# Kernel optimization log

Measured on AMD Instinct MI355X. Metric: run time of the kernel, lower is better.

## Reference

```python
import jax, jax.numpy as jnp
import numpy as np

B, L, H, OUT = 128, 256, 512, 256


def setup_inputs() -> dict:
    key = jax.random.key(0)
    ks = jax.random.split(key, 13)
    s = 1.0 / np.sqrt(H)
    u = lambda k, shape: jax.random.uniform(k, shape, jnp.float32, -s, s)
    C = jax.random.normal(ks[0], (L, H), jnp.float32)
    # strictly increasing observation times per sample
    dt0 = jax.random.uniform(ks[1], (B, L, 1), jnp.float32)
    t = jnp.cumsum(dt0, axis=1)
    mask = jax.random.randint(ks[2], (B, L, H), 0, 2).astype(jnp.int32)
    # GRU-D parameters: fused gate weights [z | r | candidate]
    Wx = u(ks[3], (H, 3 * H))   # input -> gates
    Wh = u(ks[4], (H, 3 * H))   # hidden -> gates
    Wm = u(ks[5], (H, 3 * H))   # mask  -> gates
    b = u(ks[6], (3 * H,))
    w_gx = u(ks[7], (H,))       # diagonal input-decay weight
    b_gx = u(ks[8], (H,))
    W_gh = u(ks[9], (H, H))     # hidden-decay weight
    b_gh = u(ks[10], (H,))
    W_out = u(ks[11], (H, OUT))
    b_out = u(ks[12], (OUT,))
    return dict(C=C, t=t, mask=mask, Wx=Wx, Wh=Wh, Wm=Wm, b=b, w_gx=w_gx,
                b_gx=b_gx, W_gh=W_gh, b_gh=b_gh, W_out=W_out, b_out=b_out)


def _grud_decode(C, t, mask_f, Wx, Wh, Wm, b, w_gx, b_gx, W_gh, b_gh, W_out, b_out):
    Bn, Ln = t.shape[0], t.shape[1]
    Hn = C.shape[1]
    m = mask_f                                                     # (B,L,H) float 0/1
    tt = jnp.broadcast_to(t[:, :, 0:1], (Bn, Ln, Hn))              # (B,L,H)
    dt = tt - jnp.concatenate([tt[:, :1], tt[:, :-1]], axis=1)     # dt[:,0]=0
    x = jnp.broadcast_to(C[None], (Bn, Ln, Hn))
    # empirical mean of observed values per sample/feature
    x_mean = jnp.sum(m * x, axis=1) / jnp.maximum(jnp.sum(m, axis=1), 1.0)  # (B,H)

    def step(carry, inp):
        h, x_last, d_prev, m_prev = carry
        xi, mi, dti = inp                                          # xi:(H,), mi/dti:(B,H)
        # time since last observation (GRU-D delta recurrence)
        delta = dti + (1.0 - m_prev) * d_prev
        gamma_x = jnp.exp(-jnp.maximum(0.0, w_gx * delta + b_gx))  # input decay
        gamma_h = jnp.exp(-jnp.maximum(0.0, delta @ W_gh + b_gh))  # hidden decay
        x_hat = mi * xi + (1.0 - mi) * (gamma_x * x_last + (1.0 - gamma_x) * x_mean)
        h = gamma_h * h
        pre = x_hat @ Wx + mi @ Wm + b                             # (B,3H)
        zr = jax.nn.sigmoid(pre[:, :2 * Hn] + h @ Wh[:, :2 * Hn])
        z, r = zr[:, :Hn], zr[:, Hn:]
        h_tilde = jnp.tanh(pre[:, 2 * Hn:] + (r * h) @ Wh[:, 2 * Hn:])
        h_new = (1.0 - z) * h + z * h_tilde
        x_last = mi * xi + (1.0 - mi) * x_last
        return (h_new, x_last, delta, mi), h_new

    init = (jnp.zeros((Bn, Hn), C.dtype), x_mean,
            jnp.zeros((Bn, Hn), C.dtype), jnp.ones((Bn, Hn), C.dtype))
    xs = (C, jnp.transpose(m, (1, 0, 2)), jnp.transpose(dt, (1, 0, 2)))
    _, h_seq = jax.lax.scan(step, init, xs)                        # (L,B,H)
    h_seq = jnp.transpose(h_seq, (1, 0, 2))                        # (B,L,H) == permute(1,0,2)
    return h_seq @ W_out + b_out                                   # (B,L,OUT)


def reference(C, t, mask, Wx, Wh, Wm, b, w_gx, b_gx, W_gh, b_gh, W_out, b_out):
    return _grud_decode(C, t, mask.astype(C.dtype), Wx, Wh, Wm, b,
                        w_gx, b_gx, W_gh, b_gh, W_out, b_out)
```

## Files before the change

### kernel.cpp

```cpp
#include <hip/hip_runtime.h>
#include <hip/hip_bf16.h>
#include <hip/hip_fp16.h>
#include <stdint.h>

typedef short bf16x8 __attribute__((ext_vector_type(8)));
typedef unsigned short u16x8 __attribute__((ext_vector_type(8)));
typedef float f32x4  __attribute__((ext_vector_type(4)));
typedef __hip_bfloat16 bf16;

#define MFMA16(a,b,c) __builtin_amdgcn_mfma_f32_16x16x32_bf16((a),(b),(c),0,0,0)

__device__ __forceinline__ float bf2f(bf16 x){ return __bfloat162float(x); }
__device__ __forceinline__ bf16  f2bf(float x){ return __float2bfloat16(x); }
__device__ __forceinline__ short f2bs(float x){ bf16 t = __float2bfloat16(x); return *(short*)&t; }
__device__ __forceinline__ float bs2f(short s){ bf16 t; *(short*)&t = s; return __bfloat162float(t); }
__device__ __forceinline__ float h2f(unsigned short u){ __half t; *(unsigned short*)&t = u; return __half2float(t); }
__device__ __forceinline__ float sf(float x){ return (fabsf(x) < 1e30f) ? x : 0.f; }

#define NB   128
#define NL   256
#define CH   32
#define MCH  4096
#define NQ   8


__global__ void build_wcatT(const float* __restrict__ Wx, const float* __restrict__ Wm,
                            bf16* __restrict__ dst) {
    int i = blockIdx.x * 256 + threadIdx.x;
    if (i >= 1536 * 1024) return;
    int n = i >> 10, k = i & 1023;
    float v = (k < 512) ? Wx[k * 1536 + n] : Wm[(k - 512) * 1536 + n];
    dst[i] = f2bf(sf(v));
}

__global__ void transpose_f2b(const float* __restrict__ src, bf16* __restrict__ dst,
                              int R, int C) {
    int i = blockIdx.x * 256 + threadIdx.x;
    if (i >= R * C) return;
    int r = i % R, c = i / R;
    dst[i] = f2bf(sf(src[r * C + c]));
}


__global__ void xmean_kernel(const int* __restrict__ mask, const float* __restrict__ Cmat,
                             float* __restrict__ xmean) {
    int g = blockIdx.x * 256 + threadIdx.x;
    int b = g >> 9, h = g & 511;
    float s = 0.f, cnt = 0.f;
    for (int l = 0; l < NL; ++l) {
        int m = mask[(size_t)((b << 8) + l) * 512 + h];
        if (m) { s += sf(Cmat[(l << 9) + h]); cnt += 1.f; }
    }
    xmean[g] = s / fmaxf(cnt, 1.f);
}

__global__ void prep_kernel(const int* __restrict__ mask, const float* __restrict__ Cmat,
                            const float* __restrict__ t_in,
                            const float* __restrict__ w_gx, const float* __restrict__ b_gx,
                            const float* __restrict__ xmean,
                            float* __restrict__ xlastC, float* __restrict__ dprevC,
                            float* __restrict__ mprevC, float* __restrict__ tprevC,
                            bf16* __restrict__ Xcat,
                            bf16* __restrict__ Dbuf,
                            int q) {
    int g = blockIdx.x * 256 + threadIdx.x;
    int b = g >> 9, h = g & 511;
    float wg = sf(w_gx[h]), bg = sf(b_gx[h]);
    float xm = xmean[g];
    float xlast, dprev, mprev, tprev;
    if (q == 0) { xlast = xm; dprev = 0.f; mprev = 1.f; tprev = 0.f; }
    else { xlast = xlastC[g]; dprev = dprevC[g]; mprev = mprevC[g]; tprev = tprevC[g]; }
    for (int ll = 0; ll < CH; ++ll) {
        int l = q * CH + ll;
        float tc = sf(t_in[(b << 8) + l]);
        float dtv = (l == 0) ? 0.f : (tc - tprev);
        tprev = tc;
        float mi = (float)mask[(size_t)((b << 8) + l) * 512 + h];
        float delta = dtv + (1.f - mprev) * dprev;
        float gx = __expf(-fmaxf(wg * delta + bg, 0.f));
        float xi = sf(Cmat[(l << 9) + h]);
        float xh = mi * xi + (1.f - mi) * (gx * xlast + (1.f - gx) * xm);
        size_t row = (size_t)ll * 128 + b;
        Xcat[row * 1024 + h]       = f2bf(xh);
        Xcat[row * 1024 + 512 + h] = f2bf(mi);
        Dbuf[row * 512 + h]        = f2bf(delta);
        xlast = mi * xi + (1.f - mi) * xlast;
        dprev = delta; mprev = mi;
    }
    xlastC[g] = xlast; dprevC[g] = dprev; mprevC[g] = mprev; tprevC[g] = tprev;
}

template <int MODE>
__global__ __launch_bounds__(256) void gemm_bt(const bf16* __restrict__ A,
                                               const bf16* __restrict__ BT,
                                               const float* __restrict__ bias,
                                               void* __restrict__ Cout,
                                               int N, int K, int q) {
    const int nb = N >> 7;
    int bn = blockIdx.x % nb, bm = blockIdx.x / nb;
    __shared__ bf16 As[4096];
    __shared__ bf16 Bs[4096];
    int tid = threadIdx.x, lane = tid & 63, w = tid >> 6;
    int wm = w >> 1, wn = w & 1;
    int quad = lane >> 4, l15 = lane & 15;
    f32x4 acc[4][4];
    #pragma unroll
    for (int i = 0; i < 4; ++i)
        #pragma unroll
        for (int j = 0; j < 4; ++j) acc[i][j] = (f32x4){0.f, 0.f, 0.f, 0.f};

    for (int k0 = 0; k0 < K; k0 += 32) {
        bf16x8 av[2], bv[2];
        #pragma unroll
        for (int cc = 0; cc < 2; ++cc) {
            int c = tid + cc * 256;
            int row = c >> 2, kc = c & 3;
            av[cc] = *(const bf16x8*)(A  + (size_t)(bm * 128 + row) * K + k0 + kc * 8);
            bv[cc] = *(const bf16x8*)(BT + (size_t)(bn * 128 + row) * K + k0 + kc * 8);
        }
        __syncthreads();
        #pragma unroll
        for (int cc = 0; cc < 2; ++cc) {
            int c = tid + cc * 256;
            int row = c >> 2, kc = c & 3;
            *(bf16x8*)&As[(kc * 128 + row) * 8] = av[cc];
            *(bf16x8*)&Bs[(kc * 128 + row) * 8] = bv[cc];
        }
        __syncthreads();
        bf16x8 af[4], bfr[4];
        #pragma unroll
        for (int mt = 0; mt < 4; ++mt)
            af[mt] = *(const bf16x8*)&As[(quad * 128 + wm * 64 + mt * 16 + l15) * 8];
        #pragma unroll
        for (int nt = 0; nt < 4; ++nt)
            bfr[nt] = *(const bf16x8*)&Bs[(quad * 128 + wn * 64 + nt * 16 + l15) * 8];
        #pragma unroll
        for (int mt = 0; mt < 4; ++mt)
            #pragma unroll
            for (int nt = 0; nt < 4; ++nt)
                acc[mt][nt] = MFMA16(af[mt], bfr[nt], acc[mt][nt]);
    }
    int row0 = bm * 128 + wm * 64, col0 = bn * 128 + wn * 64;
    #pragma unroll
    for (int mt = 0; mt < 4; ++mt) {
        #pragma unroll
        for (int nt = 0; nt < 4; ++nt) {
            int col = col0 + nt * 16 + l15;
            float bvf = sf(bias[col]);
            #pragma unroll
            for (int r = 0; r < 4; ++r) {
                int row = row0 + mt * 16 + quad * 4 + r;
                float v = acc[mt][nt][r] + bvf;
                if (MODE == 1)
                    ((__half*)Cout)[(size_t)row * N + col] = __float2half(__expf(-fmaxf(v, 0.f)));
                else if (MODE == 2) {
                    int bb = row & 127, lloc = row >> 7;
                    ((float*)Cout)[(size_t)((bb << 8) + q * CH + lloc) * N + col] = v;
                } else
                    ((bf16*)Cout)[(size_t)row * N + col] = f2bf(v);
            }
        }
    }
}

__global__ __launch_bounds__(256, 1) void scan_kernel(
        const bf16* __restrict__ pre,
        const __half* __restrict__ gammaf,
        const bf16* __restrict__ WhT,
        bf16* __restrict__ hseq,
        float* __restrict__ hcarry,
        bf16* __restrict__ rbuf,
        bf16* __restrict__ hnbuf,
        unsigned* __restrict__ ctr) {
    int bx = blockIdx.x;
    int c = bx & 7, w = bx >> 3;
    int tid = threadIdx.x, lane = tid & 63, v = tid >> 6;
    int wi = (w << 2) | v;
    int quad = lane >> 4, l15 = lane & 15;
    __shared__ bf16 hb[16 * 520];
    __shared__ bf16 rh[16 * 520];

    bf16x8 whz[16], whr[16], whh[16];
    int col0 = wi * 16;
    #pragma unroll
    for (int kf = 0; kf < 16; ++kf) {
        int n = col0 + l15;
        whz[kf] = *(const bf16x8*)(WhT + (size_t)n * 512 + kf * 32 + quad * 8);
        whr[kf] = *(const bf16x8*)(WhT + (size_t)(512 + n) * 512 + kf * 32 + quad * 8);
        whh[kf] = *(const bf16x8*)(WhT + (size_t)(1024 + n) * 512 + kf * 32 + quad * 8);
    }

    bf16* rclu = rbuf  + (size_t)c * 16 * 512;
    bf16* hclu = hnbuf + (size_t)c * 16 * 512;
    const unsigned short* gus = (const unsigned short*)gammaf;

    for (int i = tid; i < 16 * 512; i += 256) {
        int row = i >> 9, col = i & 511;
        int brow = c * 16 + row;
        float g0 = __half2float(gammaf[(size_t)brow * 512 + col]);
        hb[row * 520 + col] = f2bf(hcarry[(size_t)brow * 512 + col] * g0);
    }
    float hfo[4];
    #pragma unroll
    for (int r = 0; r < 4; ++r) {
        int brow = c * 16 + quad * 4 + r;
        int cc = col0 + l15;
        float g0 = __half2float(gammaf[(size_t)brow * 512 + cc]);
        hfo[r] = hcarry[(size_t)brow * 512 + cc] * g0;
    }
    __syncthreads();

    unsigned* ctrA = ctr + c * 32;
    unsigned* ctrB = ctrA + 16;
    int prow = tid >> 4;
    int pcol = (tid & 15) << 5;

    for (int t = 0; t < CH; ++t) {
        unsigned tgt = 8u * (t + 1);
        bool lastt = (t == CH - 1);
        float pz[4], prr[4], ph[4], gow[4];
        #pragma unroll
        for (int r = 0; r < 4; ++r) {
            int brow = c * 16 + quad * 4 + r;
            size_t pb = ((size_t)t * 128 + brow) * 1536;
            int cc = col0 + l15;
            pz[r]  = bf2f(pre[pb + cc]);
            prr[r] = bf2f(pre[pb + 512 + cc]);
            ph[r]  = bf2f(pre[pb + 1024 + cc]);
            gow[r] = lastt ? 1.f
                   : __half2float(gammaf[((size_t)(t + 1) * 128 + brow) * 512 + cc]);
        }
        u16x8 gt[4];
        {
            size_t gb = ((size_t)(lastt ? t : t + 1) * 128 + c * 16 + prow) * 512 + pcol;
            #pragma unroll
            for (int j = 0; j < 4; ++j) gt[j] = *(const u16x8*)(gus + gb + j * 8);
        }
        f32x4 az = (f32x4){0.f,0.f,0.f,0.f}, ar = az;
        #pragma unroll
        for (int kf = 0; kf < 16; ++kf) {
            bf16x8 a = *(const bf16x8*)&hb[l15 * 520 + kf * 32 + quad * 8];
            az = MFMA16(a, whz[kf], az);
            ar = MFMA16(a, whr[kf], ar);
        }
        float zv[4];
        #pragma unroll
        for (int r = 0; r < 4; ++r) {
            zv[r] = 1.f / (1.f + __expf(-(az[r] + pz[r])));
            float rv = 1.f / (1.f + __expf(-(ar[r] + prr[r])));
            rclu[(quad * 4 + r) * 512 + col0 + l15] = f2bf(rv);
        }
        __syncthreads();
        if (tid == 0) {
            __hip_atomic_fetch_add(ctrA, 1u, __ATOMIC_RELEASE, __HIP_MEMORY_SCOPE_AGENT);
            int guard = 0;
            while (__hip_atomic_load(ctrA, __ATOMIC_RELAXED, __HIP_MEMORY_SCOPE_AGENT) < tgt
                   && ++guard < (1 << 17))
                __builtin_amdgcn_s_sleep(1);
            __threadfence();
        }
        __syncthreads();
        #pragma unroll
        for (int j = 0; j < 4; ++j) {
            bf16x8 r8 = *(const bf16x8*)&rclu[prow * 512 + pcol + j * 8];
            bf16x8 h8 = *(const bf16x8*)&hb[prow * 520 + pcol + j * 8];
            bf16x8 o;
            #pragma unroll
            for (int e = 0; e < 8; ++e) o[e] = f2bs(bs2f(r8[e]) * bs2f(h8[e]));
            *(bf16x8*)&rh[prow * 520 + pcol + j * 8] = o;
        }
        __syncthreads();
        f32x4 ah = (f32x4){0.f,0.f,0.f,0.f};
        #pragma unroll
        for (int kf = 0; kf < 16; ++kf) {
            bf16x8 a = *(const bf16x8*)&rh[l15 * 520 + kf * 32 + quad * 8];
            ah = MFMA16(a, whh[kf], ah);
        }
        #pragma unroll
        for (int r = 0; r < 4; ++r) {
            int row = quad * 4 + r;
            int brow = c * 16 + row;
            int cc = col0 + l15;
            float x = ah[r] + ph[r];
            float e = __expf(-2.f * fabsf(x));
            float th = copysignf((1.f - e) / (1.f + e), x);
            float hn = (1.f - zv[r]) * hfo[r] + zv[r] * th;
            bf16 hnb = f2bf(hn);
            hclu[row * 512 + cc] = hnb;
            hseq[((size_t)t * 128 + brow) * 512 + cc] = hnb;
            if (lastt) hcarry[(size_t)brow * 512 + cc] = hn;
            hfo[r] = hn * gow[r];
        }
        __syncthreads();
        if (tid == 0) {
            __hip_atomic_fetch_add(ctrB, 1u, __ATOMIC_RELEASE, __HIP_MEMORY_SCOPE_AGENT);
            int guard = 0;
            while (__hip_atomic_load(ctrB, __ATOMIC_RELAXED, __HIP_MEMORY_SCOPE_AGENT) < tgt
                   && ++guard < (1 << 17))
                __builtin_amdgcn_s_sleep(1);
            __threadfence();
        }
        __syncthreads();
        #pragma unroll
        for (int j = 0; j < 4; ++j) {
            bf16x8 h8 = *(const bf16x8*)&hclu[prow * 512 + pcol + j * 8];
            bf16x8 o;
            #pragma unroll
            for (int e = 0; e < 8; ++e) {
                float g = lastt ? 1.f : h2f(gt[j][e]);
                o[e] = f2bs(bs2f(h8[e]) * g);
            }
            *(bf16x8*)&hb[prow * 520 + pcol + j * 8] = o;
        }
        __syncthreads();
    }
}


extern "C" void kernel_launch(void* const* d_in, const int* in_sizes, int n_in,
                              void* d_out, int out_size, void* d_ws, size_t ws_size,
                              hipStream_t stream) {
    const float* C     = (const float*)d_in[0];
    const float* t_in  = (const float*)d_in[1];
    const int*   mask  = (const int*)d_in[2];
    const float* Wx    = (const float*)d_in[3];
    const float* Wh    = (const float*)d_in[4];
    const float* Wm    = (const float*)d_in[5];
    const float* bvec  = (const float*)d_in[6];
    const float* w_gx  = (const float*)d_in[7];
    const float* b_gx  = (const float*)d_in[8];
    const float* W_gh  = (const float*)d_in[9];
    const float* b_gh  = (const float*)d_in[10];
    const float* W_out = (const float*)d_in[11];
    const float* b_out = (const float*)d_in[12];

    char* w = (char*)d_ws;
    unsigned* ctr   = (unsigned*)(w + 0);
    float* hcarry   = (float*)(w + 16384);
    float* xmean    = (float*)(w + 278528);
    float* xlastC   = (float*)(w + 540672);
    float* dprevC   = (float*)(w + 802816);
    float* mprevC   = (float*)(w + 1064960);
    float* tprevC   = (float*)(w + 1327104);
    bf16*  wcatT    = (bf16*)(w + 1589248);
    bf16*  wghT     = (bf16*)(w + 4734976);
    bf16*  whT      = (bf16*)(w + 5259264);
    bf16*  woutT    = (bf16*)(w + 6832128);
    bf16*  Xcat     = (bf16*)(w + 7094272);
    bf16*  Dbuf     = (bf16*)(w + 15482880);
    bf16*  pre      = (bf16*)(w + 19677184);
    __half* gamma   = (__half*)(w + 32260096);
    bf16*  hseq     = (bf16*)(w + 36454400);
    bf16*  rbuf     = (bf16*)(w + 40648704);
    bf16*  hnbuf    = (bf16*)(w + 40779776);

    hipMemsetAsync(w, 0, 278528, stream);

    build_wcatT<<<6144, 256, 0, stream>>>(Wx, Wm, wcatT);
    transpose_f2b<<<1024, 256, 0, stream>>>(W_gh, wghT, 512, 512);
    transpose_f2b<<<3072, 256, 0, stream>>>(Wh, whT, 512, 1536);
    transpose_f2b<<<512, 256, 0, stream>>>(W_out, woutT, 512, 256);
    xmean_kernel<<<256, 256, 0, stream>>>(mask, C, xmean);

    for (int q = 0; q < NQ; ++q) {
        prep_kernel<<<256, 256, 0, stream>>>(mask, C, t_in, w_gx, b_gx, xmean,
                                             xlastC, dprevC, mprevC, tprevC,
                                             Xcat, Dbuf, q);
        gemm_bt<0><<<32 * 12, 256, 0, stream>>>(Xcat, wcatT, bvec, (void*)pre, 1536, 1024, q);
        gemm_bt<1><<<32 * 4, 256, 0, stream>>>(Dbuf, wghT, b_gh, (void*)gamma, 512, 512, q);
        scan_kernel<<<64, 256, 0, stream>>>(pre, gamma, whT, hseq, hcarry,
                                            rbuf, hnbuf, ctr + q * 512);
        gemm_bt<2><<<32 * 2, 256, 0, stream>>>(hseq, woutT, b_out, d_out, 256, 512, q);
    }
}
```

Measured before the change: 3.520 ms.

## Use 512-thread scan blocks and flag-based inter-block barriers per cluster

The recurrent scan kernel now runs 32 blocks of 512 threads instead of 64 blocks of 256. Each batch cluster therefore spans 4 blocks rather than 8. The shared atomic-counter barrier is replaced by per-block epoch flags that the leader thread polls, followed by an acquire load. The aim is to cut cross-block synchronisation latency and atomic contention on each of the two per-step barriers. The hseq and hcarry stores also become nontemporal. The cost is fewer workgroups in flight and more work per block in the elementwise phases.

```diff
diff --git a/kernel.cpp b/kernel.cpp
--- a/kernel.cpp
+++ b/kernel.cpp
@@ -163,7 +163,7 @@
     }
 }
 
-__global__ __launch_bounds__(256, 1) void scan_kernel(
+__global__ __launch_bounds__(512, 1) void scan_kernel(
         const bf16* __restrict__ pre,
         const __half* __restrict__ gammaf,
         const bf16* __restrict__ WhT,
@@ -175,7 +175,7 @@
     int bx = blockIdx.x;
     int c = bx & 7, w = bx >> 3;
     int tid = threadIdx.x, lane = tid & 63, v = tid >> 6;
-    int wi = (w << 2) | v;
+    int wi = (w << 3) | v;
     int quad = lane >> 4, l15 = lane & 15;
     __shared__ bf16 hb[16 * 520];
     __shared__ bf16 rh[16 * 520];
@@ -193,8 +193,10 @@
     bf16* rclu = rbuf  + (size_t)c * 16 * 512;
     bf16* hclu = hnbuf + (size_t)c * 16 * 512;
     const unsigned short* gus = (const unsigned short*)gammaf;
-
-    for (int i = tid; i < 16 * 512; i += 256) {
+    unsigned* fA = ctr + c * 64;
+    unsigned* fB = ctr + c * 64 + 32;
+
+    for (int i = tid; i < 16 * 512; i += 512) {
         int row = i >> 9, col = i & 511;
         int brow = c * 16 + row;
         float g0 = __half2float(gammaf[(size_t)brow * 512 + col]);
@@ -210,13 +212,11 @@
     }
     __syncthreads();
 
-    unsigned* ctrA = ctr + c * 32;
-    unsigned* ctrB = ctrA + 16;
-    int prow = tid >> 4;
-    int pcol = (tid & 15) << 5;
+    int prow = tid >> 5;
+    int pcol = (tid & 31) << 4;
 
     for (int t = 0; t < CH; ++t) {
-        unsigned tgt = 8u * (t + 1);
+        unsigned ep = (unsigned)(t + 1);
         bool lastt = (t == CH - 1);
         float pz[4], prr[4], ph[4], gow[4];
         #pragma unroll
@@ -230,11 +230,11 @@
             gow[r] = lastt ? 1.f
                    : __half2float(gammaf[((size_t)(t + 1) * 128 + brow) * 512 + cc]);
         }
-        u16x8 gt[4];
+        u16x8 gt[2];
         {
             size_t gb = ((size_t)(lastt ? t : t + 1) * 128 + c * 16 + prow) * 512 + pcol;
             #pragma unroll
-            for (int j = 0; j < 4; ++j) gt[j] = *(const u16x8*)(gus + gb + j * 8);
+            for (int j = 0; j < 2; ++j) gt[j] = *(const u16x8*)(gus + gb + j * 8);
         }
         f32x4 az = (f32x4){0.f,0.f,0.f,0.f}, ar = az;
         #pragma unroll
@@ -252,16 +252,22 @@
         }
         __syncthreads();
         if (tid == 0) {
-            __hip_atomic_fetch_add(ctrA, 1u, __ATOMIC_RELEASE, __HIP_MEMORY_SCOPE_AGENT);
+            __hip_atomic_store(&fA[w], ep, __ATOMIC_RELEASE, __HIP_MEMORY_SCOPE_AGENT);
             int guard = 0;
-            while (__hip_atomic_load(ctrA, __ATOMIC_RELAXED, __HIP_MEMORY_SCOPE_AGENT) < tgt
-                   && ++guard < (1 << 17))
+            for (;;) {
+                bool ok = true;
+                #pragma unroll
+                for (int j = 0; j < 4; ++j)
+                    ok &= (__hip_atomic_load(&fA[j], __ATOMIC_RELAXED,
+                                             __HIP_MEMORY_SCOPE_AGENT) >= ep);
+                if (ok || ++guard >= (1 << 17)) break;
                 __builtin_amdgcn_s_sleep(1);
-            __threadfence();
-        }
-        __syncthreads();
-        #pragma unroll
-        for (int j = 0; j < 4; ++j) {
+            }
+            (void)__hip_atomic_load(&fA[0], __ATOMIC_ACQUIRE, __HIP_MEMORY_SCOPE_AGENT);
+        }
+        __syncthreads();
+        #pragma unroll
+        for (int j = 0; j < 2; ++j) {
             bf16x8 r8 = *(const bf16x8*)&rclu[prow * 512 + pcol + j * 8];
             bf16x8 h8 = *(const bf16x8*)&hb[prow * 520 + pcol + j * 8];
             bf16x8 o;
@@ -287,22 +293,30 @@
             float hn = (1.f - zv[r]) * hfo[r] + zv[r] * th;
             bf16 hnb = f2bf(hn);
             hclu[row * 512 + cc] = hnb;
-            hseq[((size_t)t * 128 + brow) * 512 + cc] = hnb;
-            if (lastt) hcarry[(size_t)brow * 512 + cc] = hn;
+            __builtin_nontemporal_store(*(short*)&hnb,
+                (short*)&hseq[((size_t)t * 128 + brow) * 512 + cc]);
+            if (lastt)
+                __builtin_nontemporal_store(hn, &hcarry[(size_t)brow * 512 + cc]);
             hfo[r] = hn * gow[r];
         }
         __syncthreads();
         if (tid == 0) {
-            __hip_atomic_fetch_add(ctrB, 1u, __ATOMIC_RELEASE, __HIP_MEMORY_SCOPE_AGENT);
+            __hip_atomic_store(&fB[w], ep, __ATOMIC_RELEASE, __HIP_MEMORY_SCOPE_AGENT);
             int guard = 0;
-            while (__hip_atomic_load(ctrB, __ATOMIC_RELAXED, __HIP_MEMORY_SCOPE_AGENT) < tgt
-                   && ++guard < (1 << 17))
+            for (;;) {
+                bool ok = true;
+                #pragma unroll
+                for (int j = 0; j < 4; ++j)
+                    ok &= (__hip_atomic_load(&fB[j], __ATOMIC_RELAXED,
+                                             __HIP_MEMORY_SCOPE_AGENT) >= ep);
+                if (ok || ++guard >= (1 << 17)) break;
                 __builtin_amdgcn_s_sleep(1);
-            __threadfence();
-        }
-        __syncthreads();
-        #pragma unroll
-        for (int j = 0; j < 4; ++j) {
+            }
+            (void)__hip_atomic_load(&fB[0], __ATOMIC_ACQUIRE, __HIP_MEMORY_SCOPE_AGENT);
+        }
+        __syncthreads();
+        #pragma unroll
+        for (int j = 0; j < 2; ++j) {
             bf16x8 h8 = *(const bf16x8*)&hclu[prow * 512 + pcol + j * 8];
             bf16x8 o;
             #pragma unroll
@@ -368,7 +382,7 @@
                                              Xcat, Dbuf, q);
         gemm_bt<0><<<32 * 12, 256, 0, stream>>>(Xcat, wcatT, bvec, (void*)pre, 1536, 1024, q);
         gemm_bt<1><<<32 * 4, 256, 0, stream>>>(Dbuf, wghT, b_gh, (void*)gamma, 512, 512, q);
-        scan_kernel<<<64, 256, 0, stream>>>(pre, gamma, whT, hseq, hcarry,
+        scan_kernel<<<32, 512, 0, stream>>>(pre, gamma, whT, hseq, hcarry,
                                             rbuf, hnbuf, ctr + q * 512);
         gemm_bt<2><<<32 * 2, 256, 0, stream>>>(hseq, woutT, b_out, d_out, 256, 512, q);
     }
```

Measured after the change: 3.438 ms. 1.02x faster.
